# Kernel optimization log

Hardware: AMD Instinct MI355X
Metric: run time of the kernel (lower is better)

The kernel has to match this reference:

```python
import jax, jax.numpy as jnp
import numpy as np

B, H, W, C = 32, 56, 56, 192
NUM_HEADS = 6
WS = 7
SHIFT = 3
HIDDEN = 4 * C


def _relative_position_index(ws):
    coords = np.stack(np.meshgrid(np.arange(ws), np.arange(ws), indexing="ij"))  # 2,ws,ws
    coords = coords.reshape(2, -1)
    rel = coords[:, :, None] - coords[:, None, :]  # 2,N,N
    rel = rel.transpose(1, 2, 0)
    rel[:, :, 0] += ws - 1
    rel[:, :, 1] += ws - 1
    rel[:, :, 0] *= 2 * ws - 1
    return rel.sum(-1)  # N,N in [0, (2ws-1)^2)


def setup_inputs() -> dict:
    key = jax.random.key(0)
    ks = jax.random.split(key, 16)
    s = 0.02
    inp = {
        "x": jax.random.normal(ks[0], (B, H, W, C), jnp.float32),
        "norm1_g": jnp.ones((C,), jnp.float32),
        "norm1_b": jnp.zeros((C,), jnp.float32),
        "qkv_w": jax.random.normal(ks[1], (3 * C, C), jnp.float32) * s,
        "qkv_b": jnp.zeros((3 * C,), jnp.float32),
        "proj_w": jax.random.normal(ks[2], (C, C), jnp.float32) * s,
        "proj_b": jnp.zeros((C,), jnp.float32),
        "rel_bias_table": jax.random.normal(ks[3], ((2 * WS - 1) ** 2, NUM_HEADS), jnp.float32) * s,
        "norm2_g": jnp.ones((C,), jnp.float32),
        "norm2_b": jnp.zeros((C,), jnp.float32),
        "fc1_w": jax.random.normal(ks[4], (HIDDEN, C), jnp.float32) * s,
        "fc1_b": jnp.zeros((HIDDEN,), jnp.float32),
        "fc2_w": jax.random.normal(ks[5], (C, HIDDEN), jnp.float32) * s,
        "fc2_b": jnp.zeros((C,), jnp.float32),
        "rel_index": jnp.asarray(_relative_position_index(WS), jnp.int32),  # (49,49)
    }
    return inp


def _layernorm(x, g, b, eps=1e-5):
    mu = x.mean(-1, keepdims=True)
    var = ((x - mu) ** 2).mean(-1, keepdims=True)
    return (x - mu) * jax.lax.rsqrt(var + eps) * g + b


def _window_partition(x, ws):
    b, h, w, c = x.shape
    x = x.reshape(b, h // ws, ws, w // ws, ws, c)
    return x.transpose(0, 1, 3, 2, 4, 5).reshape(-1, ws * ws, c)


def _window_reverse(win, ws, b, h, w):
    c = win.shape[-1]
    x = win.reshape(b, h // ws, w // ws, ws, ws, c)
    return x.transpose(0, 1, 3, 2, 4, 5).reshape(b, h, w, c)


def reference(x, norm1_g, norm1_b, qkv_w, qkv_b, proj_w, proj_b, rel_bias_table,
              norm2_g, norm2_b, fc1_w, fc1_b, fc2_w, fc2_b, rel_index):
    shortcut = x
    xn = _layernorm(x, norm1_g, norm1_b)
    xs = jnp.roll(xn, (-SHIFT, -SHIFT), axis=(1, 2))
    win = _window_partition(xs, WS)  # (nW*B, 49, C)
    nw, n, c = win.shape
    hd = c // NUM_HEADS
    qkv = win @ qkv_w.T + qkv_b  # (nw, n, 3C)
    qkv = qkv.reshape(nw, n, 3, NUM_HEADS, hd).transpose(2, 0, 3, 1, 4)
    q, k, v = qkv[0], qkv[1], qkv[2]  # (nw, heads, n, hd)
    q = q * (hd ** -0.5)
    attn = jnp.einsum("whnd,whmd->whnm", q, k)
    bias = rel_bias_table[rel_index.reshape(-1)].reshape(n, n, NUM_HEADS).transpose(2, 0, 1)
    attn = jax.nn.softmax(attn + bias[None], axis=-1)
    out = jnp.einsum("whnm,whmd->whnd", attn, v)
    out = out.transpose(0, 2, 1, 3).reshape(nw, n, c)
    out = out @ proj_w.T + proj_b
    xs = _window_reverse(out, WS, x.shape[0], x.shape[1], x.shape[2])
    xa = jnp.roll(xs, (SHIFT, SHIFT), axis=(1, 2))
    x = shortcut + xa
    xm = _layernorm(x, norm2_g, norm2_b)
    xm = jax.nn.gelu(xm @ fc1_w.T + fc1_b, approximate=False)
    xm = xm @ fc2_w.T + fc2_b
    return x + xm
```

## Files before the change

### kernel.cpp

```cpp
#include <hip/hip_runtime.h>
#include <hip/hip_bf16.h>

#define CC 192
#define NHEADS 6
#define HDIM 32
#define NTOK 49
#define NWIN 2048
#define MTOK 100352
#define HIDDEN 768

typedef __hip_bfloat16 bf16;
typedef __attribute__((ext_vector_type(8))) short short8;
typedef __attribute__((ext_vector_type(4))) float f32x4;

__global__ __launch_bounds__(256) void k_wconv(
    const float* __restrict__ qw, const float* __restrict__ pw,
    const float* __restrict__ f1, const float* __restrict__ f2,
    bf16* __restrict__ o) {
  int i = blockIdx.x * 256 + threadIdx.x;
  if (i < 110592) o[i] = __float2bfloat16(qw[i]);
  else if (i < 147456) o[i] = __float2bfloat16(pw[i - 110592]);
  else if (i < 294912) o[i] = __float2bfloat16(f1[i - 147456]);
  else if (i < 442368) o[i] = __float2bfloat16(f2[i - 294912]);
}

__global__ __launch_bounds__(256) void k_bias(
    const float* __restrict__ table, const int* __restrict__ ridx,
    float* __restrict__ bias6) {
  int i = blockIdx.x * 256 + threadIdx.x;
  if (i >= 6 * 2401) return;
  int h = i / 2401, e = i - h * 2401;
  bias6[i] = table[ridx[e] * NHEADS + h];
}

template <int MODE, int NT, int KC, int MF>
__global__ __launch_bounds__(256) void k_gemm_areg(
    const void* __restrict__ Ap, const bf16* __restrict__ W,
    const float* __restrict__ bias, void* __restrict__ out0,
    const void* __restrict__ aux, const float* __restrict__ lng,
    const float* __restrict__ lnb) {
  constexpr int K = KC * 192;
  constexpr int N = NT * 64;
  __shared__ bf16 Bs[2][64 * 192];
  const int tid = threadIdx.x;
  const int wave = tid >> 6, lane = tid & 63;
  const int grp = lane >> 4, rA = lane & 15;
  const int cq = grp, cn = rA;
  const int m0 = blockIdx.x * (MF * 64);
  const int mrow = m0 + wave * (MF * 16);

  short8 areg[MF][KC * 6];
  if constexpr (MODE == 1 || MODE == 3) {
#pragma unroll
    for (int mt = 0; mt < MF; ++mt) {
      const bf16* arow =
          (const bf16*)Ap + (size_t)(mrow + mt * 16 + rA) * K + grp * 8;
#pragma unroll
      for (int kt = 0; kt < KC * 6; ++kt)
        areg[mt][kt] = *(const short8*)(arow + kt * 32);
    }
  } else {
#pragma unroll
    for (int mt = 0; mt < MF; ++mt) {
      int m = mrow + mt * 16 + rA;
      const float* rowp;
      if constexpr (MODE == 0) {
        int w = m / 49, n = m - w * 49;
        int b = w >> 6, wrem = w & 63;
        int hi = wrem >> 3, wi = wrem & 7;
        int ii = n / 7, jj = n - ii * 7;
        int hs = hi * 7 + ii + 3; if (hs >= 56) hs -= 56;
        int wsc = wi * 7 + jj + 3; if (wsc >= 56) wsc -= 56;
        rowp = (const float*)Ap + (size_t)((b * 56 + hs) * 56 + wsc) * CC;
      } else {
        rowp = (const float*)Ap + (size_t)m * CC;
      }
      f32x4 xv[12];
#pragma unroll
      for (int kt = 0; kt < 6; ++kt) {
        xv[2 * kt]     = *(const f32x4*)(rowp + kt * 32 + grp * 8);
        xv[2 * kt + 1] = *(const f32x4*)(rowp + kt * 32 + grp * 8 + 4);
      }
      float s = 0.0f;
#pragma unroll
      for (int i = 0; i < 12; ++i)
#pragma unroll
        for (int j = 0; j < 4; ++j) s += xv[i][j];
      s += __shfl_xor(s, 16, 64);
      s += __shfl_xor(s, 32, 64);
      float mu = s * (1.0f / 192.0f);
      float q = 0.0f;
#pragma unroll
      for (int i = 0; i < 12; ++i)
#pragma unroll
        for (int j = 0; j < 4; ++j) {
          float d = xv[i][j] - mu;
          q += d * d;
        }
      q += __shfl_xor(q, 16, 64);
      q += __shfl_xor(q, 32, 64);
      float inv = rsqrtf(q * (1.0f / 192.0f) + 1e-5f);
#pragma unroll
      for (int kt = 0; kt < 6; ++kt) {
        short8 t;
#pragma unroll
        for (int j = 0; j < 8; ++j) {
          int col = kt * 32 + grp * 8 + j;
          float xval = xv[2 * kt + (j >> 2)][j & 3];
          float val = (xval - mu) * inv * lng[col] + lnb[col];
          bf16 hb = __float2bfloat16(val);
          t[j] = *reinterpret_cast<short*>(&hb);
        }
        areg[mt][kt] = t;
      }
    }
  }

  int rowoff[MF][4];
  if constexpr (MODE == 1) {
#pragma unroll
    for (int mt = 0; mt < MF; ++mt)
#pragma unroll
      for (int r = 0; r < 4; ++r) {
        int m = mrow + mt * 16 + cq * 4 + r;
        int w = m / 49, rr = m - w * 49;
        int b = w >> 6, wrem = w & 63;
        int hi = wrem >> 3, wi = wrem & 7;
        int ii = rr / 7, jj = rr - ii * 7;
        int hd = hi * 7 + ii + 3; if (hd >= 56) hd -= 56;
        int wd = wi * 7 + jj + 3; if (wd >= 56) wd -= 56;
        rowoff[mt][r] = ((b * 56 + hd) * 56 + wd) * CC;
      }
  }

  auto stage = [&](int buf, int nt, int kc) {
#pragma unroll
    for (int i = 0; i < 6; ++i) {
      int c = i * 256 + tid;
      int row = c / 24;
      int cbl = ((c - row * 24) * 16) ^ ((row & 7) << 4);
      const char* src = (const char*)W +
          (size_t)(nt * 64 + row) * (K * 2) + kc * 384 + cbl;
      __builtin_amdgcn_global_load_lds(
          (const __attribute__((address_space(1))) void*)src,
          (__attribute__((address_space(3))) void*)((char*)&Bs[buf][0] + c * 16),
          16, 0, 0);
    }
  };
  stage(0, 0, 0);

  f32x4 acc[MF][4];
#pragma unroll
  for (int s = 0; s < NT * KC; ++s) {
    const int nt = s / KC, kc = s - nt * KC;
    const int cur = s & 1;
    __syncthreads();
    if (s + 1 < NT * KC) stage(cur ^ 1, (s + 1) / KC, (s + 1) % KC);
    if (kc == 0) {
#pragma unroll
      for (int mt = 0; mt < MF; ++mt)
#pragma unroll
        for (int ntf = 0; ntf < 4; ++ntf)
          acc[mt][ntf] = (f32x4){0.f, 0.f, 0.f, 0.f};
    }
#pragma unroll
    for (int kt = 0; kt < 6; ++kt) {
      short8 b[4];
#pragma unroll
      for (int ntf = 0; ntf < 4; ++ntf) {
        int row = ntf * 16 + rA;
        int phys = row * 384 + ((kt * 64 + grp * 16) ^ ((row & 7) << 4));
        b[ntf] = *(const short8*)((const char*)&Bs[cur][0] + phys);
      }
#pragma unroll
      for (int mt = 0; mt < MF; ++mt)
#pragma unroll
        for (int ntf = 0; ntf < 4; ++ntf)
          acc[mt][ntf] = __builtin_amdgcn_mfma_f32_16x16x32_bf16(
              areg[mt][kc * 6 + kt], b[ntf], acc[mt][ntf], 0, 0, 0);
    }
    if (kc == KC - 1) {
      const int n0t = nt * 64;
      float bi[4];
#pragma unroll
      for (int ntf = 0; ntf < 4; ++ntf) bi[ntf] = bias[n0t + ntf * 16 + cn];
#pragma unroll
      for (int mt = 0; mt < MF; ++mt) {
#pragma unroll
        for (int r = 0; r < 4; ++r) {
          const int m = mrow + mt * 16 + cq * 4 + r;
#pragma unroll
          for (int ntf = 0; ntf < 4; ++ntf) {
            const int n = n0t + ntf * 16 + cn;
            float v = acc[mt][ntf][r] + bi[ntf];
            if constexpr (MODE == 0) {
              ((bf16*)out0)[(size_t)m * N + n] = __float2bfloat16(v);
            } else if constexpr (MODE == 2) {
              float u2 = 2.0f * v * (0.7978845608f + 0.0356774081f * v * v);
              float t = 1.0f - 2.0f / (1.0f + __expf(u2));
              float ge = 0.5f * v * (1.0f + t);
              ((bf16*)out0)[(size_t)m * N + n] = __float2bfloat16(ge);
            } else if constexpr (MODE == 1) {
              float res = ((const float*)aux)[(size_t)rowoff[mt][r] + n];
              ((float*)out0)[(size_t)rowoff[mt][r] + n] = v + res;
            } else {
              float res = ((const float*)aux)[(size_t)m * CC + n];
              ((float*)out0)[(size_t)m * CC + n] = v + res;
            }
          }
        }
      }
    }
  }
}

__global__ __launch_bounds__(256) void k_attn_mfma(
    const bf16* __restrict__ qk, const float* __restrict__ bias6,
    bf16* __restrict__ ao) {
  __shared__ bf16 P[4][64 * 72];
  __shared__ bf16 VT[4][32 * 72];
  const int wave = threadIdx.x >> 6, lane = threadIdx.x & 63;
  const int wh = blockIdx.x * 4 + wave;
  const int w = wh / NHEADS, h = wh - w * NHEADS;
  const int rA = lane & 15, kq = (lane >> 4) * 8;
  const int grp = lane >> 4;

  const bf16* qbase = qk + (size_t)(w * 49) * 576 + h * HDIM + kq;

  short8 aq[4], bk[4], vrow[4];
#pragma unroll
  for (int t = 0; t < 4; ++t) {
    const bf16* rp = qbase + (size_t)(t * 16 + rA) * 576;
    aq[t] = *(const short8*)(rp);
    bk[t] = *(const short8*)(rp + 192);
    vrow[t] = *(const short8*)(rp + 384);
  }

  f32x4 S[4][4] = {};
#pragma unroll
  for (int mt = 0; mt < 4; ++mt)
#pragma unroll
    for (int nt = 0; nt < 4; ++nt)
      S[mt][nt] = __builtin_amdgcn_mfma_f32_16x16x32_bf16(
          aq[mt], bk[nt], S[mt][nt], 0, 0, 0);

  bf16* Vw = VT[wave];
  const bf16 zero = __float2bfloat16(0.0f);
#pragma unroll
  for (int t = 0; t < 4; ++t) {
    int tok = t * 16 + rA;
#pragma unroll
    for (int j = 0; j < 8; ++j)
      Vw[(kq + j) * 72 + tok] = (tok < 49) ? ((const bf16*)&vrow[t])[j] : zero;
  }

  const float scale = 0.17677669529663687f;
  const float* bh = bias6 + h * 2401;
  float rs[4][4];
  bf16* Pw = P[wave];
#pragma unroll
  for (int mt = 0; mt < 4; ++mt) {
#pragma unroll
    for (int r = 0; r < 4; ++r) {
      int row = mt * 16 + grp * 4 + r;
      float val[4];
#pragma unroll
      for (int nt = 0; nt < 4; ++nt) {
        int c = nt * 16 + rA;
        float bv = (row < 49 && c < 49) ? bh[row * 49 + c] : 0.0f;
        val[nt] = (c < 49) ? (S[mt][nt][r] * scale + bv) : -1e30f;
      }
      float mx = fmaxf(fmaxf(val[0], val[1]), fmaxf(val[2], val[3]));
      for (int m2 = 1; m2 < 16; m2 <<= 1) mx = fmaxf(mx, __shfl_xor(mx, m2, 64));
      float sum = 0.0f;
#pragma unroll
      for (int nt = 0; nt < 4; ++nt) {
        float e = __expf(val[nt] - mx);
        val[nt] = e;
        sum += e;
      }
      for (int m2 = 1; m2 < 16; m2 <<= 1) sum += __shfl_xor(sum, m2, 64);
      rs[mt][r] = 1.0f / sum;
#pragma unroll
      for (int nt = 0; nt < 4; ++nt)
        Pw[row * 72 + nt * 16 + rA] = __float2bfloat16(val[nt]);
    }
  }
  __syncthreads();

  short8 bv[2][2];
#pragma unroll
  for (int ks = 0; ks < 2; ++ks)
#pragma unroll
    for (int nt = 0; nt < 2; ++nt)
      bv[ks][nt] = *(const short8*)&Vw[(nt * 16 + rA) * 72 + ks * 32 + kq];
  f32x4 O[4][2] = {};
#pragma unroll
  for (int mt = 0; mt < 4; ++mt) {
    short8 ap0 = *(const short8*)&Pw[(mt * 16 + rA) * 72 + kq];
    short8 ap1 = *(const short8*)&Pw[(mt * 16 + rA) * 72 + 32 + kq];
#pragma unroll
    for (int nt = 0; nt < 2; ++nt) {
      O[mt][nt] = __builtin_amdgcn_mfma_f32_16x16x32_bf16(ap0, bv[0][nt],
                                                          O[mt][nt], 0, 0, 0);
      O[mt][nt] = __builtin_amdgcn_mfma_f32_16x16x32_bf16(ap1, bv[1][nt],
                                                          O[mt][nt], 0, 0, 0);
    }
  }
#pragma unroll
  for (int mt = 0; mt < 4; ++mt) {
#pragma unroll
    for (int r = 0; r < 4; ++r) {
      int m = mt * 16 + grp * 4 + r;
      if (m < 49) {
        bf16* orow = ao + (size_t)(w * 49 + m) * CC + h * HDIM;
#pragma unroll
        for (int nt = 0; nt < 2; ++nt)
          orow[nt * 16 + rA] = __float2bfloat16(O[mt][nt][r] * rs[mt][r]);
      }
    }
  }
}

extern "C" void kernel_launch(void* const* d_in, const int* in_sizes, int n_in,
                              void* d_out, int out_size, void* d_ws, size_t ws_size,
                              hipStream_t stream) {
  const float* x        = (const float*)d_in[0];
  const float* norm1_g  = (const float*)d_in[1];
  const float* norm1_b  = (const float*)d_in[2];
  const float* qkv_w    = (const float*)d_in[3];
  const float* qkv_b    = (const float*)d_in[4];
  const float* proj_w   = (const float*)d_in[5];
  const float* proj_b   = (const float*)d_in[6];
  const float* rel_tab  = (const float*)d_in[7];
  const float* norm2_g  = (const float*)d_in[8];
  const float* norm2_b  = (const float*)d_in[9];
  const float* fc1_w    = (const float*)d_in[10];
  const float* fc1_b    = (const float*)d_in[11];
  const float* fc2_w    = (const float*)d_in[12];
  const float* fc2_b    = (const float*)d_in[13];
  const int*   rel_idx  = (const int*)d_in[14];
  float* out = (float*)d_out;

  const size_t SZ_QKB = 115605504ull;
  const size_t SZ_HBF = 154140672ull;
  const size_t SZ_AO  = 38535168ull;
  const size_t SZ_WB  = 884736ull;
  const size_t SZ_B6  = 57624ull;
  const bool fullM = ws_size >= SZ_HBF + SZ_AO + SZ_WB + SZ_B6;

  char* ws = (char*)d_ws;
  bf16 *qkb, *ao, *wbuf, *hbuf;
  float* bias6;
  if (fullM) {
    qkb   = (bf16*)ws;
    hbuf  = (bf16*)ws;
    ao    = (bf16*)(ws + SZ_HBF);
    wbuf  = (bf16*)(ws + SZ_HBF + SZ_AO);
    bias6 = (float*)(ws + SZ_HBF + SZ_AO + SZ_WB);
  } else {
    qkb   = (bf16*)ws;
    hbuf  = (bf16*)ws;
    ao    = (bf16*)(ws + SZ_QKB);
    wbuf  = (bf16*)(ws + SZ_QKB + SZ_AO);
    bias6 = (float*)(ws + SZ_QKB + SZ_AO + SZ_WB);
  }
  float* x1 = out;
  bf16* wq = wbuf;
  bf16* wp = wbuf + 110592;
  bf16* w1 = wbuf + 147456;
  bf16* w2 = wbuf + 294912;

  k_wconv<<<1728, 256, 0, stream>>>(qkv_w, proj_w, fc1_w, fc2_w, wbuf);
  k_bias<<<57, 256, 0, stream>>>(rel_tab, rel_idx, bias6);
  k_gemm_areg<0, 9, 1, 1><<<MTOK / 64, 256, 0, stream>>>(
      x, wq, qkv_b, qkb, nullptr, norm1_g, norm1_b);
  k_attn_mfma<<<NWIN * NHEADS / 4, 256, 0, stream>>>(qkb, bias6, ao);
  k_gemm_areg<1, 3, 1, 2><<<MTOK / 128, 256, 0, stream>>>(
      ao, wp, proj_b, x1, x, nullptr, nullptr);
  if (fullM) {
    k_gemm_areg<2, 12, 1, 1><<<MTOK / 64, 256, 0, stream>>>(
        x1, w1, fc1_b, hbuf, nullptr, norm2_g, norm2_b);
    k_gemm_areg<3, 3, 4, 1><<<MTOK / 64, 256, 0, stream>>>(
        hbuf, w2, fc2_b, out, x1, nullptr, nullptr);
  } else {
    const int MH = MTOK / 2;
    for (int h = 0; h < 2; ++h) {
      size_t mo = (size_t)h * MH;
      k_gemm_areg<2, 12, 1, 1><<<MH / 64, 256, 0, stream>>>(
          x1 + mo * CC, w1, fc1_b, hbuf, nullptr, norm2_g, norm2_b);
      k_gemm_areg<3, 3, 4, 1><<<MH / 64, 256, 0, stream>>>(
          hbuf, w2, fc2_b, out + mo * CC, x1 + mo * CC, nullptr, nullptr);
    }
  }
}
```

Baseline: 473.5 us.

## Fuse LN2, fc1+GELU and fc2 into a single MLP kernel

Replaces the separate fc1 (with LayerNorm and GELU) and fc2 GEMM launches with one kernel. Each block keeps 64 rows, computes the hidden activations in 64-column chunks into LDS, and accumulates fc2 output in registers, so the 154 MB bf16 hidden buffer is never written to or read from global memory. The cost is that the W1/W2 chunk loads are serialized with extra barriers per chunk, and each wave holds 12 accumulators, which raises register pressure and may lower occupancy.

```diff
diff --git a/kernel.cpp b/kernel.cpp
--- a/kernel.cpp
+++ b/kernel.cpp
@@ -50,7 +50,7 @@
   const int mrow = m0 + wave * (MF * 16);
 
   short8 areg[MF][KC * 6];
-  if constexpr (MODE == 1 || MODE == 3) {
+  if constexpr (MODE == 1) {
 #pragma unroll
     for (int mt = 0; mt < MF; ++mt) {
       const bf16* arow =
@@ -63,18 +63,14 @@
 #pragma unroll
     for (int mt = 0; mt < MF; ++mt) {
       int m = mrow + mt * 16 + rA;
-      const float* rowp;
-      if constexpr (MODE == 0) {
-        int w = m / 49, n = m - w * 49;
-        int b = w >> 6, wrem = w & 63;
-        int hi = wrem >> 3, wi = wrem & 7;
-        int ii = n / 7, jj = n - ii * 7;
-        int hs = hi * 7 + ii + 3; if (hs >= 56) hs -= 56;
-        int wsc = wi * 7 + jj + 3; if (wsc >= 56) wsc -= 56;
-        rowp = (const float*)Ap + (size_t)((b * 56 + hs) * 56 + wsc) * CC;
-      } else {
-        rowp = (const float*)Ap + (size_t)m * CC;
-      }
+      int w = m / 49, n = m - w * 49;
+      int b = w >> 6, wrem = w & 63;
+      int hi = wrem >> 3, wi = wrem & 7;
+      int ii = n / 7, jj = n - ii * 7;
+      int hs = hi * 7 + ii + 3; if (hs >= 56) hs -= 56;
+      int wsc = wi * 7 + jj + 3; if (wsc >= 56) wsc -= 56;
+      const float* rowp =
+          (const float*)Ap + (size_t)((b * 56 + hs) * 56 + wsc) * CC;
       f32x4 xv[12];
 #pragma unroll
       for (int kt = 0; kt < 6; ++kt) {
@@ -195,21 +191,165 @@
             float v = acc[mt][ntf][r] + bi[ntf];
             if constexpr (MODE == 0) {
               ((bf16*)out0)[(size_t)m * N + n] = __float2bfloat16(v);
-            } else if constexpr (MODE == 2) {
-              float u2 = 2.0f * v * (0.7978845608f + 0.0356774081f * v * v);
-              float t = 1.0f - 2.0f / (1.0f + __expf(u2));
-              float ge = 0.5f * v * (1.0f + t);
-              ((bf16*)out0)[(size_t)m * N + n] = __float2bfloat16(ge);
-            } else if constexpr (MODE == 1) {
+            } else {
               float res = ((const float*)aux)[(size_t)rowoff[mt][r] + n];
               ((float*)out0)[(size_t)rowoff[mt][r] + n] = v + res;
-            } else {
-              float res = ((const float*)aux)[(size_t)m * CC + n];
-              ((float*)out0)[(size_t)m * CC + n] = v + res;
             }
           }
         }
       }
+    }
+  }
+}
+
+__global__ __launch_bounds__(256) void k_mlp(
+    const float* __restrict__ x1, const bf16* __restrict__ W1,
+    const bf16* __restrict__ W2, const float* __restrict__ b1,
+    const float* __restrict__ b2, float* __restrict__ out,
+    const float* __restrict__ lng, const float* __restrict__ lnb) {
+  __shared__ bf16 Bs[2][64 * 192];
+  __shared__ bf16 Hl[4][16 * 72];
+  const int tid = threadIdx.x;
+  const int wave = tid >> 6, lane = tid & 63;
+  const int grp = lane >> 4, rA = lane & 15;
+  const int mrow = blockIdx.x * 64 + wave * 16;
+  char* hb = (char*)&Hl[wave][0];
+
+  short8 areg[6];
+  {
+    const float* rowp = x1 + (size_t)(mrow + rA) * CC;
+    f32x4 xv[12];
+#pragma unroll
+    for (int kt = 0; kt < 6; ++kt) {
+      xv[2 * kt]     = *(const f32x4*)(rowp + kt * 32 + grp * 8);
+      xv[2 * kt + 1] = *(const f32x4*)(rowp + kt * 32 + grp * 8 + 4);
+    }
+    float s = 0.0f;
+#pragma unroll
+    for (int i = 0; i < 12; ++i)
+#pragma unroll
+      for (int j = 0; j < 4; ++j) s += xv[i][j];
+    s += __shfl_xor(s, 16, 64);
+    s += __shfl_xor(s, 32, 64);
+    float mu = s * (1.0f / 192.0f);
+    float q = 0.0f;
+#pragma unroll
+    for (int i = 0; i < 12; ++i)
+#pragma unroll
+      for (int j = 0; j < 4; ++j) {
+        float d = xv[i][j] - mu;
+        q += d * d;
+      }
+    q += __shfl_xor(q, 16, 64);
+    q += __shfl_xor(q, 32, 64);
+    float inv = rsqrtf(q * (1.0f / 192.0f) + 1e-5f);
+#pragma unroll
+    for (int kt = 0; kt < 6; ++kt) {
+      short8 t;
+#pragma unroll
+      for (int j = 0; j < 8; ++j) {
+        int col = kt * 32 + grp * 8 + j;
+        float xval = xv[2 * kt + (j >> 2)][j & 3];
+        float val = (xval - mu) * inv * lng[col] + lnb[col];
+        bf16 hbv = __float2bfloat16(val);
+        t[j] = *reinterpret_cast<short*>(&hbv);
+      }
+      areg[kt] = t;
+    }
+  }
+
+  auto stage1 = [&](int c) {
+#pragma unroll
+    for (int i = 0; i < 6; ++i) {
+      int cc = i * 256 + tid;
+      int row = cc / 24;
+      int cbl = ((cc - row * 24) * 16) ^ ((row & 7) << 4);
+      const char* src = (const char*)W1 + (size_t)(c * 64 + row) * 384 + cbl;
+      __builtin_amdgcn_global_load_lds(
+          (const __attribute__((address_space(1))) void*)src,
+          (__attribute__((address_space(3))) void*)((char*)&Bs[0][0] + cc * 16),
+          16, 0, 0);
+    }
+  };
+  auto stage2 = [&](int c) {
+#pragma unroll
+    for (int i = 0; i < 6; ++i) {
+      int cc = i * 256 + tid;
+      int row = cc >> 3, slot = cc & 7;
+      int cbl = (slot * 16) ^ ((row & 7) << 4);
+      const char* src = (const char*)W2 + (size_t)row * 1536 + c * 128 + cbl;
+      __builtin_amdgcn_global_load_lds(
+          (const __attribute__((address_space(1))) void*)src,
+          (__attribute__((address_space(3))) void*)((char*)&Bs[1][0] + cc * 16),
+          16, 0, 0);
+    }
+  };
+
+  f32x4 acc2[12];
+#pragma unroll
+  for (int nf = 0; nf < 12; ++nf) acc2[nf] = (f32x4){0.f, 0.f, 0.f, 0.f};
+
+  stage1(0);
+  for (int c = 0; c < 12; ++c) {
+    __syncthreads();
+    stage2(c);
+    f32x4 fa[4] = {};
+#pragma unroll
+    for (int kt = 0; kt < 6; ++kt) {
+      short8 bfr[4];
+#pragma unroll
+      for (int ntf = 0; ntf < 4; ++ntf) {
+        int row = ntf * 16 + rA;
+        int phys = row * 384 + ((kt * 64 + grp * 16) ^ ((row & 7) << 4));
+        bfr[ntf] = *(const short8*)((const char*)&Bs[0][0] + phys);
+      }
+#pragma unroll
+      for (int ntf = 0; ntf < 4; ++ntf)
+        fa[ntf] = __builtin_amdgcn_mfma_f32_16x16x32_bf16(
+            areg[kt], bfr[ntf], fa[ntf], 0, 0, 0);
+    }
+#pragma unroll
+    for (int ntf = 0; ntf < 4; ++ntf) {
+      float b1v = b1[c * 64 + ntf * 16 + rA];
+#pragma unroll
+      for (int r = 0; r < 4; ++r) {
+        float v = fa[ntf][r] + b1v;
+        float u2 = 2.0f * v * (0.7978845608f + 0.0356774081f * v * v);
+        float t = 1.0f - 2.0f / (1.0f + __expf(u2));
+        float ge = 0.5f * v * (1.0f + t);
+        int row = grp * 4 + r;
+        int byte = (row * 144 + (ntf * 16 + rA) * 2) ^ ((row & 8) << 1);
+        *(bf16*)(hb + byte) = __float2bfloat16(ge);
+      }
+    }
+    __syncthreads();
+    if (c + 1 < 12) stage1(c + 1);
+    short8 a2[2];
+#pragma unroll
+    for (int kt2 = 0; kt2 < 2; ++kt2)
+      a2[kt2] = *(const short8*)(
+          hb + ((rA * 144 + grp * 16 + kt2 * 64) ^ ((rA & 8) << 1)));
+#pragma unroll
+    for (int nf = 0; nf < 12; ++nf) {
+      int row = nf * 16 + rA;
+      int sw = (row & 7) << 4;
+      short8 bw0 = *(const short8*)(
+          (const char*)&Bs[1][0] + row * 128 + ((grp * 16) ^ sw));
+      short8 bw1 = *(const short8*)(
+          (const char*)&Bs[1][0] + row * 128 + ((64 + grp * 16) ^ sw));
+      acc2[nf] = __builtin_amdgcn_mfma_f32_16x16x32_bf16(a2[0], bw0, acc2[nf], 0, 0, 0);
+      acc2[nf] = __builtin_amdgcn_mfma_f32_16x16x32_bf16(a2[1], bw1, acc2[nf], 0, 0, 0);
+    }
+  }
+
+#pragma unroll
+  for (int nf = 0; nf < 12; ++nf) {
+    float b2v = b2[nf * 16 + rA];
+#pragma unroll
+    for (int r = 0; r < 4; ++r) {
+      int m = mrow + grp * 4 + r;
+      size_t idx = (size_t)m * CC + nf * 16 + rA;
+      out[idx] = out[idx] + acc2[nf][r] + b2v;
     }
   }
 }
@@ -342,30 +482,12 @@
   const int*   rel_idx  = (const int*)d_in[14];
   float* out = (float*)d_out;
 
-  const size_t SZ_QKB = 115605504ull;
-  const size_t SZ_HBF = 154140672ull;
-  const size_t SZ_AO  = 38535168ull;
-  const size_t SZ_WB  = 884736ull;
-  const size_t SZ_B6  = 57624ull;
-  const bool fullM = ws_size >= SZ_HBF + SZ_AO + SZ_WB + SZ_B6;
-
   char* ws = (char*)d_ws;
-  bf16 *qkb, *ao, *wbuf, *hbuf;
-  float* bias6;
-  if (fullM) {
-    qkb   = (bf16*)ws;
-    hbuf  = (bf16*)ws;
-    ao    = (bf16*)(ws + SZ_HBF);
-    wbuf  = (bf16*)(ws + SZ_HBF + SZ_AO);
-    bias6 = (float*)(ws + SZ_HBF + SZ_AO + SZ_WB);
-  } else {
-    qkb   = (bf16*)ws;
-    hbuf  = (bf16*)ws;
-    ao    = (bf16*)(ws + SZ_QKB);
-    wbuf  = (bf16*)(ws + SZ_QKB + SZ_AO);
-    bias6 = (float*)(ws + SZ_QKB + SZ_AO + SZ_WB);
-  }
-  float* x1 = out;
+  bf16*  qkb   = (bf16*)ws;
+  bf16*  ao    = (bf16*)(ws + 115605504);
+  bf16*  wbuf  = (bf16*)(ws + 154140672);
+  float* bias6 = (float*)(ws + 155025408);
+  float* x1    = out;
   bf16* wq = wbuf;
   bf16* wp = wbuf + 110592;
   bf16* w1 = wbuf + 147456;
@@ -378,19 +500,6 @@
   k_attn_mfma<<<NWIN * NHEADS / 4, 256, 0, stream>>>(qkb, bias6, ao);
   k_gemm_areg<1, 3, 1, 2><<<MTOK / 128, 256, 0, stream>>>(
       ao, wp, proj_b, x1, x, nullptr, nullptr);
-  if (fullM) {
-    k_gemm_areg<2, 12, 1, 1><<<MTOK / 64, 256, 0, stream>>>(
-        x1, w1, fc1_b, hbuf, nullptr, norm2_g, norm2_b);
-    k_gemm_areg<3, 3, 4, 1><<<MTOK / 64, 256, 0, stream>>>(
-        hbuf, w2, fc2_b, out, x1, nullptr, nullptr);
-  } else {
-    const int MH = MTOK / 2;
-    for (int h = 0; h < 2; ++h) {
-      size_t mo = (size_t)h * MH;
-      k_gemm_areg<2, 12, 1, 1><<<MH / 64, 256, 0, stream>>>(
-          x1 + mo * CC, w1, fc1_b, hbuf, nullptr, norm2_g, norm2_b);
-      k_gemm_areg<3, 3, 4, 1><<<MH / 64, 256, 0, stream>>>(
-          hbuf, w2, fc2_b, out + mo * CC, x1 + mo * CC, nullptr, nullptr);
-    }
-  }
+  k_mlp<<<MTOK / 64, 256, 0, stream>>>(
+      x1, w1, w2, fc1_b, fc2_b, out, norm2_g, norm2_b);
 }
```

Measured after the change: 451.9 us. 4.6% less time.
